# Performance work log

Measured on AMD Instinct MI355X. Metric: run time of the kernel, lower is better.

## Reference

```python
import jax, jax.numpy as jnp
import numpy as np

N = 16      # manifold_dim
H = 128     # hidden_dim
B = 256     # batch
EPS = 1e-6


def setup_inputs() -> dict:
    key = jax.random.key(0)
    ks = jax.random.split(key, 14)
    def w(k, shape):
        fan_in = shape[0]
        return jax.random.uniform(k, shape, jnp.float32, -1.0, 1.0) / np.sqrt(fan_in)
    return {
        "points": jax.random.normal(ks[0], (B, N), jnp.float32),
        # metric network: N -> H -> N*N
        "mW1": w(ks[1], (N, H)), "mb1": jnp.zeros((H,), jnp.float32),
        "mW2": w(ks[2], (H, N * N)), "mb2": jnp.zeros((N * N,), jnp.float32),
        # christoffel network: 3 -> H -> 1
        "cW1": w(ks[3], (3, H)), "cb1": jnp.zeros((H,), jnp.float32),
        "cW2": w(ks[4], (H, 1)), "cb2": jnp.zeros((1,), jnp.float32),
        # ricci network: 4N -> 2H -> N*N
        "rW1": w(ks[5], (4 * N, 2 * H)), "rb1": jnp.zeros((2 * H,), jnp.float32),
        "rW2": w(ks[6], (2 * H, N * N)), "rb2": jnp.zeros((N * N,), jnp.float32),
    }


def reference(points, mW1, mb1, mW2, mb2, cW1, cb1, cW2, cb2, rW1, rb1, rW2, rb2):
    b = points.shape[0]
    n = N
    # ---- metric: (b, n, n) ----
    mh = jax.nn.relu(points @ mW1 + mb1)
    metric = (mh @ mW2 + mb2).reshape(b, n, n)
    metric = metric + EPS * jnp.eye(n, dtype=metric.dtype)
    metric = 0.5 * (metric + jnp.swapaxes(metric, -2, -1))

    # ---- christoffel: vectorized over all (i,j,k) triples ----
    # inputs per triple: [metric_ij, metric_jk, metric_ki]
    m_ij = jnp.broadcast_to(metric[:, :, :, None], (b, n, n, n))
    m_jk = jnp.broadcast_to(metric[:, None, :, :], (b, n, n, n))
    mT = jnp.swapaxes(metric, -2, -1)  # mT[b,i,k] = metric[b,k,i]
    m_ki = jnp.broadcast_to(mT[:, :, None, :], (b, n, n, n))
    ch_in = jnp.stack([m_ij, m_jk, m_ki], axis=-1)        # (b,n,n,n,3)
    ch_h = jnp.tanh(ch_in @ cW1 + cb1)                    # (b,n,n,n,H)
    christoffel = (ch_h @ cW2 + cb2)[..., 0]              # (b,n,n,n)

    # ---- ricci: vectorized over all (i,j) pairs ----
    p_b = jnp.broadcast_to(points[:, None, None, :], (b, n, n, n))
    m_i = jnp.broadcast_to(metric[:, :, None, :], (b, n, n, n))
    m_j = jnp.broadcast_to(metric[:, None, :, :], (b, n, n, n))
    r_in = jnp.concatenate([p_b, m_i, m_j, christoffel], axis=-1)  # (b,n,n,4n)
    r_h = jax.nn.relu(r_in @ rW1 + rb1)                   # (b,n,n,2H)
    r_out = (r_h @ rW2 + rb2).reshape(b, n, n, n, n)      # (b,i,j,n,n)
    r_out = 0.5 * (r_out + jnp.swapaxes(r_out, -1, -2))
    ricci = r_out.sum(axis=(1, 2)) / (n * n)              # (b,n,n)
    return ricci
```

## Files before the change

kernel.cpp:

```cpp
#include <hip/hip_runtime.h>
#include <hip/hip_bf16.h>

#define NDIM 16
#define HDIM 128
#define BATCH 256
#define EPS_D 1e-6f

__global__ __launch_bounds__(256) void metric_kernel(
    const float* __restrict__ points,
    const float* __restrict__ mW1, const float* __restrict__ mb1,
    const float* __restrict__ mW2, const float* __restrict__ mb2,
    float* __restrict__ metric) {
  int b = blockIdx.x;
  int t = threadIdx.x;
  __shared__ float p[16];
  __shared__ float mh[128];
  __shared__ float raw[256];
  if (t < 16) p[t] = points[b * 16 + t];
  __syncthreads();
  if (t < 128) {
    float acc = mb1[t];
#pragma unroll
    for (int k = 0; k < 16; ++k) acc = fmaf(p[k], mW1[k * 128 + t], acc);
    mh[t] = fmaxf(acc, 0.f);
  }
  __syncthreads();
  {
    float acc = mb2[t];
#pragma unroll 8
    for (int h = 0; h < 128; ++h) acc = fmaf(mh[h], mW2[h * 256 + t], acc);
    raw[t] = acc;
  }
  __syncthreads();
  int i = t >> 4, j = t & 15;
  float v = 0.5f * (raw[i * 16 + j] + raw[j * 16 + i]);
  if (i == j) v += EPS_D;
  metric[b * 256 + t] = v;
}

__global__ __launch_bounds__(256) void proj_kernel(
    const float* __restrict__ points,
    const float* __restrict__ metric,
    const float* __restrict__ rW1, const float* __restrict__ rb1,
    float* __restrict__ A1, float* __restrict__ Mi, float* __restrict__ Mj) {
  int b = blockIdx.x;
  int h = threadIdx.x;
  __shared__ float p[16];
  __shared__ float M[256];
  if (h < 16) p[h] = points[b * 16 + h];
  M[h] = metric[b * 256 + h];
  __syncthreads();
  float a = rb1[h];
#pragma unroll
  for (int r = 0; r < 16; ++r) a = fmaf(p[r], rW1[r * 256 + h], a);
  A1[b * 256 + h] = a;
  for (int i = 0; i < 16; ++i) {
    float mi = 0.f, mj = 0.f;
#pragma unroll
    for (int c = 0; c < 16; ++c) {
      float m = M[i * 16 + c];
      mi = fmaf(m, rW1[(16 + c) * 256 + h], mi);
      mj = fmaf(m, rW1[(32 + c) * 256 + h], mj);
    }
    Mi[(b * 16 + i) * 256 + h] = mi;
    Mj[(b * 16 + i) * 256 + h] = mj;
  }
}

__global__ __launch_bounds__(256) void chr_kernel(
    const float* __restrict__ metric,
    const float* __restrict__ cW1, const float* __restrict__ cb1,
    const float* __restrict__ cW2, const float* __restrict__ cb2,
    const float* __restrict__ rW1,
    const float* __restrict__ A1, const float* __restrict__ Mi,
    const float* __restrict__ Mj,
    float* __restrict__ H2i) {
  int bi = blockIdx.x;
  int b = bi >> 4, i = bi & 15;
  int t = threadIdx.x;
  __shared__ float M[256];
  __shared__ float ch[256];
  __shared__ float w1[384];
  __shared__ float b1[128];
  __shared__ float w2[128];
  __shared__ float rc[16 * 256];
  M[t] = metric[b * 256 + t];
  if (t < 128) {
    b1[t] = cb1[t];
    w2[t] = cW2[t];
  }
  if (t < 192) {
    w1[t] = cW1[t];
    w1[t + 192] = cW1[t + 192];
  }
#pragma unroll
  for (int k = 0; k < 16; ++k) rc[k * 256 + t] = rW1[(48 + k) * 256 + t];
  __syncthreads();

  {
    int j = t >> 4, k = t & 15;
    float x0 = M[i * 16 + j];
    float x1 = M[j * 16 + k];
    float x2 = M[k * 16 + i];
    float acc = cb2[0];
#pragma unroll 4
    for (int h = 0; h < 128; ++h) {
      float pre = fmaf(x0, w1[h], fmaf(x1, w1[128 + h], fmaf(x2, w1[256 + h], b1[h])));
      acc = fmaf(tanhf(pre), w2[h], acc);
    }
    ch[t] = acc;
  }
  __syncthreads();

  {
    int h = t;
    float base = A1[b * 256 + h] + Mi[bi * 256 + h];
    float hacc = 0.f;
    for (int jj = 0; jj < 16; ++jj) {
      float cp = 0.f;
#pragma unroll
      for (int kk = 0; kk < 16; ++kk)
        cp = fmaf(ch[jj * 16 + kk], rc[kk * 256 + h], cp);
      float v = base + Mj[(b * 16 + jj) * 256 + h] + cp;
      hacc += fmaxf(v, 0.f);
    }
    H2i[bi * 256 + h] = hacc;
  }
}

__global__ __launch_bounds__(256) void final_kernel(
    const float* __restrict__ H2i,
    const float* __restrict__ rW2, const float* __restrict__ rb2,
    float* __restrict__ out) {
  int b = blockIdx.x;
  int t = threadIdx.x;
  __shared__ float G[256];
  __shared__ float T[256];
  float g = 0.f;
#pragma unroll
  for (int i = 0; i < 16; ++i) g += H2i[(b * 16 + i) * 256 + t];
  G[t] = g;
  __syncthreads();
  float acc = 256.f * rb2[t];
#pragma unroll 8
  for (int h = 0; h < 256; ++h) acc = fmaf(G[h], rW2[h * 256 + t], acc);
  T[t] = acc * (1.f / 256.f);
  __syncthreads();
  int k = t >> 4, l = t & 15;
  out[b * 256 + t] = 0.5f * (T[k * 16 + l] + T[l * 16 + k]);
}

extern "C" void kernel_launch(void* const* d_in, const int* in_sizes, int n_in,
                              void* d_out, int out_size, void* d_ws, size_t ws_size,
                              hipStream_t stream) {
  const float* points = (const float*)d_in[0];
  const float* mW1 = (const float*)d_in[1];
  const float* mb1 = (const float*)d_in[2];
  const float* mW2 = (const float*)d_in[3];
  const float* mb2 = (const float*)d_in[4];
  const float* cW1 = (const float*)d_in[5];
  const float* cb1 = (const float*)d_in[6];
  const float* cW2 = (const float*)d_in[7];
  const float* cb2 = (const float*)d_in[8];
  const float* rW1 = (const float*)d_in[9];
  const float* rb1 = (const float*)d_in[10];
  const float* rW2 = (const float*)d_in[11];
  const float* rb2 = (const float*)d_in[12];
  float* out = (float*)d_out;

  float* ws = (float*)d_ws;
  float* metric = ws;
  float* A1 = metric + 65536;
  float* Mi = A1 + 65536;
  float* Mj = Mi + 1048576;
  float* H2i = Mj + 1048576;

  metric_kernel<<<BATCH, 256, 0, stream>>>(points, mW1, mb1, mW2, mb2, metric);
  proj_kernel<<<BATCH, 256, 0, stream>>>(points, metric, rW1, rb1, A1, Mi, Mj);
  chr_kernel<<<BATCH * NDIM, 256, 0, stream>>>(metric, cW1, cb1, cW2, cb2, rW1,
                                               A1, Mi, Mj, H2i);
  final_kernel<<<BATCH, 256, 0, stream>>>(H2i, rW2, rb2, out);
}
```

Baseline: 162.5 us.

## Fuse metric and projection kernels, use fast exp tanh, halve chr block size

Merges metric and proj kernels into one launch that keeps the metric in shared memory. In the Christoffel kernel, tanhf is replaced with an exp2/rcp formula that has cW1 and cb1 prescaled by 2*log2(e). The block shrinks to 128 threads, each handling two (j,k) triples and two hidden units. The rc weight slice now lives in registers instead of a 16KB shared array, which cuts shared-memory use and raises occupancy. The fast tanh gives up a little accuracy and may overflow for large inputs, though exp2 saturating to inf still yields tanh=1.

```diff
diff --git a/kernel.cpp b/kernel.cpp
--- a/kernel.cpp
+++ b/kernel.cpp
@@ -6,16 +6,19 @@
 #define BATCH 256
 #define EPS_D 1e-6f
 
-__global__ __launch_bounds__(256) void metric_kernel(
+__global__ __launch_bounds__(256) void metric_proj_kernel(
     const float* __restrict__ points,
     const float* __restrict__ mW1, const float* __restrict__ mb1,
     const float* __restrict__ mW2, const float* __restrict__ mb2,
-    float* __restrict__ metric) {
+    const float* __restrict__ rW1, const float* __restrict__ rb1,
+    float* __restrict__ metric,
+    float* __restrict__ A1, float* __restrict__ Mi, float* __restrict__ Mj) {
   int b = blockIdx.x;
   int t = threadIdx.x;
   __shared__ float p[16];
   __shared__ float mh[128];
   __shared__ float raw[256];
+  __shared__ float M[256];
   if (t < 16) p[t] = points[b * 16 + t];
   __syncthreads();
   if (t < 128) {
@@ -32,42 +35,42 @@
     raw[t] = acc;
   }
   __syncthreads();
-  int i = t >> 4, j = t & 15;
-  float v = 0.5f * (raw[i * 16 + j] + raw[j * 16 + i]);
-  if (i == j) v += EPS_D;
-  metric[b * 256 + t] = v;
-}
-
-__global__ __launch_bounds__(256) void proj_kernel(
-    const float* __restrict__ points,
-    const float* __restrict__ metric,
-    const float* __restrict__ rW1, const float* __restrict__ rb1,
-    float* __restrict__ A1, float* __restrict__ Mi, float* __restrict__ Mj) {
-  int b = blockIdx.x;
-  int h = threadIdx.x;
-  __shared__ float p[16];
-  __shared__ float M[256];
-  if (h < 16) p[h] = points[b * 16 + h];
-  M[h] = metric[b * 256 + h];
-  __syncthreads();
-  float a = rb1[h];
-#pragma unroll
-  for (int r = 0; r < 16; ++r) a = fmaf(p[r], rW1[r * 256 + h], a);
-  A1[b * 256 + h] = a;
-  for (int i = 0; i < 16; ++i) {
-    float mi = 0.f, mj = 0.f;
+  {
+    int i = t >> 4, j = t & 15;
+    float v = 0.5f * (raw[i * 16 + j] + raw[j * 16 + i]);
+    if (i == j) v += EPS_D;
+    M[t] = v;
+    metric[b * 256 + t] = v;
+  }
+  __syncthreads();
+  {
+    int h = t;
+    float wB[16], wC[16];
 #pragma unroll
     for (int c = 0; c < 16; ++c) {
-      float m = M[i * 16 + c];
-      mi = fmaf(m, rW1[(16 + c) * 256 + h], mi);
-      mj = fmaf(m, rW1[(32 + c) * 256 + h], mj);
-    }
-    Mi[(b * 16 + i) * 256 + h] = mi;
-    Mj[(b * 16 + i) * 256 + h] = mj;
-  }
-}
-
-__global__ __launch_bounds__(256) void chr_kernel(
+      wB[c] = rW1[(16 + c) * 256 + h];
+      wC[c] = rW1[(32 + c) * 256 + h];
+    }
+    float a = rb1[h];
+#pragma unroll
+    for (int r = 0; r < 16; ++r) a = fmaf(p[r], rW1[r * 256 + h], a);
+    A1[b * 256 + h] = a;
+#pragma unroll 2
+    for (int i = 0; i < 16; ++i) {
+      float mi = 0.f, mj = 0.f;
+#pragma unroll
+      for (int c = 0; c < 16; ++c) {
+        float m = M[i * 16 + c];
+        mi = fmaf(m, wB[c], mi);
+        mj = fmaf(m, wC[c], mj);
+      }
+      Mi[(b * 16 + i) * 256 + h] = mi;
+      Mj[(b * 16 + i) * 256 + h] = mj;
+    }
+  }
+}
+
+__global__ __launch_bounds__(128) void chr_kernel(
     const float* __restrict__ metric,
     const float* __restrict__ cW1, const float* __restrict__ cb1,
     const float* __restrict__ cW2, const float* __restrict__ cb2,
@@ -79,52 +82,73 @@
   int b = bi >> 4, i = bi & 15;
   int t = threadIdx.x;
   __shared__ float M[256];
+  __shared__ float4 q[128];
+  __shared__ float w2[128];
   __shared__ float ch[256];
-  __shared__ float w1[384];
-  __shared__ float b1[128];
-  __shared__ float w2[128];
-  __shared__ float rc[16 * 256];
   M[t] = metric[b * 256 + t];
-  if (t < 128) {
-    b1[t] = cb1[t];
+  M[t + 128] = metric[b * 256 + t + 128];
+  {
+    const float S = 2.8853900817779268f;
+    q[t] = make_float4(S * cW1[t], S * cW1[128 + t], S * cW1[256 + t],
+                       S * cb1[t]);
     w2[t] = cW2[t];
   }
-  if (t < 192) {
-    w1[t] = cW1[t];
-    w1[t + 192] = cW1[t + 192];
-  }
-#pragma unroll
-  for (int k = 0; k < 16; ++k) rc[k * 256 + t] = rW1[(48 + k) * 256 + t];
-  __syncthreads();
-
-  {
-    int j = t >> 4, k = t & 15;
-    float x0 = M[i * 16 + j];
-    float x1 = M[j * 16 + k];
-    float x2 = M[k * 16 + i];
-    float acc = cb2[0];
+  __syncthreads();
+
+  {
+    int j0 = t >> 4, k0 = t & 15;
+    int j1 = j0 + 8, k1 = k0;
+    float x00 = M[i * 16 + j0], x01 = M[j0 * 16 + k0], x02 = M[k0 * 16 + i];
+    float x10 = M[i * 16 + j1], x11 = M[j1 * 16 + k1], x12 = M[k1 * 16 + i];
+    float c2 = cb2[0];
+    float acc0 = c2, acc1 = c2;
 #pragma unroll 4
     for (int h = 0; h < 128; ++h) {
-      float pre = fmaf(x0, w1[h], fmaf(x1, w1[128 + h], fmaf(x2, w1[256 + h], b1[h])));
-      acc = fmaf(tanhf(pre), w2[h], acc);
-    }
-    ch[t] = acc;
-  }
-  __syncthreads();
-
-  {
-    int h = t;
-    float base = A1[b * 256 + h] + Mi[bi * 256 + h];
-    float hacc = 0.f;
+      float4 Q = q[h];
+      float w = w2[h];
+      float pre0 = fmaf(x00, Q.x, fmaf(x01, Q.y, fmaf(x02, Q.z, Q.w)));
+      float pre1 = fmaf(x10, Q.x, fmaf(x11, Q.y, fmaf(x12, Q.z, Q.w)));
+      float e0 = __builtin_amdgcn_exp2f(pre0);
+      float e1 = __builtin_amdgcn_exp2f(pre1);
+      float r0 = __builtin_amdgcn_rcpf(e0 + 1.f);
+      float r1 = __builtin_amdgcn_rcpf(e1 + 1.f);
+      float th0 = fmaf(-2.f, r0, 1.f);
+      float th1 = fmaf(-2.f, r1, 1.f);
+      acc0 = fmaf(th0, w, acc0);
+      acc1 = fmaf(th1, w, acc1);
+    }
+    ch[t] = acc0;
+    ch[t + 128] = acc1;
+  }
+  __syncthreads();
+
+  {
+    int h0 = t, h1 = t + 128;
+    float rc0[16], rc1[16];
+#pragma unroll
+    for (int kk = 0; kk < 16; ++kk) {
+      rc0[kk] = rW1[(48 + kk) * 256 + h0];
+      rc1[kk] = rW1[(48 + kk) * 256 + h1];
+    }
+    float base0 = A1[b * 256 + h0] + Mi[bi * 256 + h0];
+    float base1 = A1[b * 256 + h1] + Mi[bi * 256 + h1];
+    float hacc0 = 0.f, hacc1 = 0.f;
+#pragma unroll 2
     for (int jj = 0; jj < 16; ++jj) {
-      float cp = 0.f;
-#pragma unroll
-      for (int kk = 0; kk < 16; ++kk)
-        cp = fmaf(ch[jj * 16 + kk], rc[kk * 256 + h], cp);
-      float v = base + Mj[(b * 16 + jj) * 256 + h] + cp;
-      hacc += fmaxf(v, 0.f);
-    }
-    H2i[bi * 256 + h] = hacc;
+      float cp0 = 0.f, cp1 = 0.f;
+#pragma unroll
+      for (int kk = 0; kk < 16; ++kk) {
+        float c = ch[jj * 16 + kk];
+        cp0 = fmaf(c, rc0[kk], cp0);
+        cp1 = fmaf(c, rc1[kk], cp1);
+      }
+      float mj0 = Mj[(b * 16 + jj) * 256 + h0];
+      float mj1 = Mj[(b * 16 + jj) * 256 + h1];
+      hacc0 += fmaxf(base0 + mj0 + cp0, 0.f);
+      hacc1 += fmaxf(base1 + mj1 + cp1, 0.f);
+    }
+    H2i[bi * 256 + h0] = hacc0;
+    H2i[bi * 256 + h1] = hacc1;
   }
 }
 
@@ -175,9 +199,9 @@
   float* Mj = Mi + 1048576;
   float* H2i = Mj + 1048576;
 
-  metric_kernel<<<BATCH, 256, 0, stream>>>(points, mW1, mb1, mW2, mb2, metric);
-  proj_kernel<<<BATCH, 256, 0, stream>>>(points, metric, rW1, rb1, A1, Mi, Mj);
-  chr_kernel<<<BATCH * NDIM, 256, 0, stream>>>(metric, cW1, cb1, cW2, cb2, rW1,
+  metric_proj_kernel<<<BATCH, 256, 0, stream>>>(points, mW1, mb1, mW2, mb2,
+                                                rW1, rb1, metric, A1, Mi, Mj);
+  chr_kernel<<<BATCH * NDIM, 128, 0, stream>>>(metric, cW1, cb1, cW2, cb2, rW1,
                                                A1, Mi, Mj, H2i);
   final_kernel<<<BATCH, 256, 0, stream>>>(H2i, rW2, rb2, out);
 }
```

Result: faster. 145.7 us (-10.4%).
